# Kernel tuning notes

Hardware: AMD Instinct MI355X
Metric: run time of the kernel (lower is better)

## Reference

```python
import jax, jax.numpy as jnp
import numpy as np

KS = [3, 3, 7, 7, 11, 11, 21, 21]  # TEXT_KERNEL_SIZES
KMAX = 21
H = 8
D_MODEL = 1024
D_H = D_MODEL // H
R = 4
B = 2
N = 4096


def _extract_windows_1d(xh, k):
    # xh: (B, n, d_h) -> windows: (B, n, k, d_h), zero-padded, stride 1
    pad = k // 2
    xp = jnp.pad(xh, ((0, 0), (pad, pad), (0, 0)))
    idx = jnp.arange(xh.shape[1])[:, None] + jnp.arange(k)[None, :]  # (n, k)
    return xp[:, idx]  # (B, n, k, d_h)


def setup_inputs() -> dict:
    key = jax.random.key(0)
    ks = jax.random.split(key, 10)
    s = 0.02
    return {
        "x": jax.random.normal(ks[0], (B, N, D_MODEL), dtype=jnp.float32),
        "W_in": jax.random.normal(ks[1], (D_MODEL, D_MODEL), dtype=jnp.float32) * s,
        "b_in": jnp.zeros((D_MODEL,), dtype=jnp.float32),
        "W_out": jax.random.normal(ks[2], (D_MODEL, D_MODEL), dtype=jnp.float32) * (0.02 / np.sqrt(2.0 * 8)),
        "b_out": jnp.zeros((D_MODEL,), dtype=jnp.float32),
        "Wc": jax.random.normal(ks[3], (H, D_H, R), dtype=jnp.float32) * s,  # per-token coeff proj
        "A": jax.random.normal(ks[4], (H, R, KMAX), dtype=jnp.float32) * s,  # rank -> kernel-pos factor (padded to KMAX)
        "V": jax.random.normal(ks[5], (H, R, D_H), dtype=jnp.float32) * s,   # rank -> channel factor
        "base": jax.random.normal(ks[6], (H, KMAX, D_H), dtype=jnp.float32) * s,  # static kernel (padded)
        "alphas": jnp.zeros((H,), dtype=jnp.float32),  # sigmoid gate params
    }


def reference(x, W_in, b_in, W_out, b_out, Wc, A, V, base, alphas):
    Bsz, n, d = x.shape
    x_proj = x @ W_in.T + b_in                        # (B, n, d_model)
    x_heads = x_proj.reshape(Bsz, n, H, D_H)          # (B, n, H, d_h)
    head_outs = []
    for h in range(H):
        k = KS[h]
        x_h = x_heads[:, :, h, :]                     # (B, n, d_h)
        # Factored per-token kernel generation
        c = x_h @ Wc[h]                               # (B, n, R)
        dyn = jnp.einsum('bnr,rk,rd->bnkd', c, A[h, :, :k], V[h])  # (B, n, k, d_h)
        alpha = jax.nn.sigmoid(alphas[h])
        K_hat = alpha * dyn + (1.0 - alpha) * base[h, :k][None, None]  # (B, n, k, d_h)
        windows = _extract_windows_1d(x_h, k)         # (B, n, k, d_h)
        o_h = jnp.einsum('bnkd,bnkd->bnd', K_hat, windows)
        head_outs.append(o_h)
    concat = jnp.concatenate(head_outs, axis=-1)      # (B, n, d_model)
    return concat @ W_out.T + b_out
```

## Files before the change

kernel.cpp:

```cpp
#include <hip/hip_runtime.h>
#include <stdint.h>

typedef __bf16 bf16;
typedef __bf16 bf16x8 __attribute__((ext_vector_type(8)));
typedef float f32x4 __attribute__((ext_vector_type(4)));

#define AS1 __attribute__((address_space(1)))
#define AS3 __attribute__((address_space(3)))

__device__ __forceinline__ void gload_lds16(const void* g, void* l) {
    __builtin_amdgcn_global_load_lds((const AS1 uint32_t*)g, (AS3 uint32_t*)l, 16, 0, 0);
}

#define BM 128
#define BN 64
#define BK 64

template <typename OT>
__global__ __launch_bounds__(256, 4) void gemm_nt(
    const bf16* __restrict__ A, const bf16* __restrict__ B,
    const float* __restrict__ bias, OT* __restrict__ C,
    int M, int N, int K)
{
    __shared__ bf16 smA[BM * BK];
    __shared__ bf16 smB[BN * BK];

    const int tid  = threadIdx.x;
    const int wave = tid >> 6;
    const int lane = tid & 63;
    const int wm = (wave >> 1) * 64;
    const int wn = (wave & 1) * 32;
    const int rowA0 = blockIdx.x * BM;
    const int rowB0 = blockIdx.y * BN;

    f32x4 acc[4][2] = {};

    const int g  = lane >> 4;
    const int rm = lane & 15;

    for (int k0 = 0; k0 < K; k0 += BK) {
        #pragma unroll
        for (int i = 0; i < 4; ++i) {
            int slot = i * 256 + tid;
            int row  = slot >> 3;
            int kg   = slot & 7;
            int kd   = kg ^ ((row >> 1) & 7);
            gload_lds16(A + (size_t)(rowA0 + row) * K + k0 + kd * 8, &smA[slot * 8]);
        }
        #pragma unroll
        for (int i = 0; i < 2; ++i) {
            int slot = i * 256 + tid;
            int row  = slot >> 3;
            int kg   = slot & 7;
            int kd   = kg ^ ((row >> 1) & 7);
            gload_lds16(B + (size_t)(rowB0 + row) * K + k0 + kd * 8, &smB[slot * 8]);
        }
        __syncthreads();

        #pragma unroll
        for (int s = 0; s < 2; ++s) {
            bf16x8 af[4], bfr[2];
            #pragma unroll
            for (int mi = 0; mi < 4; ++mi) {
                int row  = wm + mi * 16 + rm;
                int slot = row * 8 + ((s * 4 + g) ^ ((row >> 1) & 7));
                af[mi] = *(const bf16x8*)&smA[slot * 8];
            }
            #pragma unroll
            for (int ni = 0; ni < 2; ++ni) {
                int row  = wn + ni * 16 + rm;
                int slot = row * 8 + ((s * 4 + g) ^ ((row >> 1) & 7));
                bfr[ni] = *(const bf16x8*)&smB[slot * 8];
            }
            #pragma unroll
            for (int mi = 0; mi < 4; ++mi)
                #pragma unroll
                for (int ni = 0; ni < 2; ++ni)
                    acc[mi][ni] = __builtin_amdgcn_mfma_f32_16x16x32_bf16(
                        af[mi], bfr[ni], acc[mi][ni], 0, 0, 0);
        }
        __syncthreads();
    }

    const int quad = lane >> 4;
    #pragma unroll
    for (int ni = 0; ni < 2; ++ni) {
        int col = rowB0 + wn + ni * 16 + rm;
        float bcol = bias[col];
        #pragma unroll
        for (int mi = 0; mi < 4; ++mi) {
            #pragma unroll
            for (int r = 0; r < 4; ++r) {
                int rowc = rowA0 + wm + mi * 16 + quad * 4 + r;
                C[(size_t)rowc * N + col] = (OT)(acc[mi][ni][r] + bcol);
            }
        }
    }
}

__global__ void cast_all_kernel(const float* __restrict__ x, bf16* __restrict__ xb,
                                const float* __restrict__ wi, bf16* __restrict__ wib,
                                const float* __restrict__ wo, bf16* __restrict__ wob)
{
    const int NX8 = (2 * 4096 * 1024) / 8;
    const int NW8 = (1024 * 1024) / 8;
    int i = blockIdx.x * 256 + threadIdx.x;
    const float* in; bf16* out; int idx;
    if (i < NX8)            { in = x;  out = xb;  idx = i; }
    else if (i < NX8 + NW8) { in = wi; out = wib; idx = i - NX8; }
    else                    { in = wo; out = wob; idx = i - NX8 - NW8; }
    const float4* p = (const float4*)in;
    float4 a = p[2 * idx], b = p[2 * idx + 1];
    bf16x8 o;
    o[0] = (bf16)a.x; o[1] = (bf16)a.y; o[2] = (bf16)a.z; o[3] = (bf16)a.w;
    o[4] = (bf16)b.x; o[5] = (bf16)b.y; o[6] = (bf16)b.z; o[7] = (bf16)b.w;
    *(bf16x8*)(out + 8 * idx) = o;
}

__global__ __launch_bounds__(256) void c_compute(
    const bf16* __restrict__ xpb, const float* __restrict__ Wc,
    float* __restrict__ cbuf)
{
    const int wave = threadIdx.x >> 6, lane = threadIdx.x & 63;
    const int row  = blockIdx.x * 4 + wave;
    const int h    = lane >> 3;
    const int d0   = (lane & 7) * 16;

    const bf16* xr = xpb + (size_t)row * 1024 + lane * 16;
    bf16x8 v0 = *(const bf16x8*)xr;
    bf16x8 v1 = *(const bf16x8*)(xr + 8);
    float p0 = 0.f, p1 = 0.f, p2 = 0.f, p3 = 0.f;
    #pragma unroll
    for (int i = 0; i < 16; ++i) {
        float xv = (i < 8) ? (float)v0[i & 7] : (float)v1[i & 7];
        float4 wr = *(const float4*)(Wc + h * 512 + (d0 + i) * 4);
        p0 += xv * wr.x; p1 += xv * wr.y; p2 += xv * wr.z; p3 += xv * wr.w;
    }
    #pragma unroll
    for (int off = 1; off <= 4; off <<= 1) {
        p0 += __shfl_xor(p0, off);
        p1 += __shfl_xor(p1, off);
        p2 += __shfl_xor(p2, off);
        p3 += __shfl_xor(p3, off);
    }
    if ((lane & 7) == 0) {
        float4 o = {p0, p1, p2, p3};
        *(float4*)(cbuf + (size_t)row * 32 + h * 4) = o;
    }
}

__constant__ int KS_c[8] = {3, 3, 7, 7, 11, 11, 21, 21};

template <int K>
__device__ __forceinline__ void mix_body5(
    int h, int tid, int r0, const bf16* __restrict__ xpb,
    const float* __restrict__ cbuf, const float* __restrict__ Aw,
    const float* __restrict__ Vw, const float* __restrict__ basew,
    float alpha, bf16* __restrict__ y, bf16* sx, float* sB)
{
    constexpr int T   = 8;
    constexpr int pad = K / 2;
    constexpr int R   = 16 + 2 * pad;
    constexpr int SX  = R * 16;
    constexpr int SB  = K * 32;

    #pragma unroll
    for (int p = 0; p < (SX + 255) / 256; ++p) {
        int slot = p * 256 + tid;
        if (slot < SX) {
            int lrow = slot >> 4;
            int grow = min(max(r0 - pad + lrow, 0), 8191);
            gload_lds16(xpb + (size_t)grow * 1024 + h * 128 + (slot & 15) * 8,
                        sx + slot * 8);
        }
    }
    #pragma unroll
    for (int p = 0; p < (SB + 255) / 256; ++p) {
        int slot = p * 256 + tid;
        if (slot < SB)
            gload_lds16(basew + h * 2688 + slot * 4, sB + slot * 4);
    }
    __syncthreads();

    const int d   = tid & 127;
    const int sub = tid >> 7;
    const int lr0 = sub * 8;
    const int nb  = (r0 & 4095) + sub * 8;

    float w[T + K - 1];
    #pragma unroll
    for (int j = 0; j < T + K - 1; ++j) {
        int nl = nb + j - pad;
        float v = (float)sx[(lr0 + j) * 128 + d];
        w[j] = (nl >= 0 && nl < 4096) ? v : 0.f;
    }

    float s0[T] = {}, s1[T] = {}, s2[T] = {}, s3[T] = {}, tv[T] = {};
    const float* Ah = Aw + h * 84;
    #pragma unroll
    for (int j = 0; j < K; ++j) {
        float a0 = Ah[j], a1 = Ah[21 + j], a2 = Ah[42 + j], a3 = Ah[63 + j];
        float bbj = sB[j * 128 + d];
        #pragma unroll
        for (int t = 0; t < T; ++t) {
            float x = w[t + j];
            s0[t] += a0 * x; s1[t] += a1 * x;
            s2[t] += a2 * x; s3[t] += a3 * x;
            tv[t] += bbj * x;
        }
    }

    float v0 = Vw[h * 512 + d],       v1 = Vw[h * 512 + 128 + d];
    float v2 = Vw[h * 512 + 256 + d], v3 = Vw[h * 512 + 384 + d];
    #pragma unroll
    for (int t = 0; t < T; ++t) {
        int rowo = r0 + sub * 8 + t;
        float4 c4 = *(const float4*)(cbuf + (size_t)rowo * 32 + h * 4);
        float o = alpha * (c4.x * v0 * s0[t] + c4.y * v1 * s1[t] +
                           c4.z * v2 * s2[t] + c4.w * v3 * s3[t])
                + (1.f - alpha) * tv[t];
        y[(size_t)rowo * 1024 + h * 128 + d] = (bf16)o;
    }
}

__global__ __launch_bounds__(256, 4) void head_mix5(
    const bf16* __restrict__ xpb, const float* __restrict__ cbuf,
    const float* __restrict__ Aw, const float* __restrict__ Vw,
    const float* __restrict__ basew, const float* __restrict__ alphas,
    bf16* __restrict__ y)
{
    __shared__ __align__(16) bf16  sx[36 * 128];
    __shared__ __align__(16) float sB[21 * 128];
    const int h  = blockIdx.y;
    const int r0 = blockIdx.x * 16;
    const float alpha = 1.f / (1.f + __expf(-alphas[h]));

    switch (KS_c[h]) {
        case 3:  mix_body5<3 >(h, threadIdx.x, r0, xpb, cbuf, Aw, Vw, basew, alpha, y, sx, sB); break;
        case 7:  mix_body5<7 >(h, threadIdx.x, r0, xpb, cbuf, Aw, Vw, basew, alpha, y, sx, sB); break;
        case 11: mix_body5<11>(h, threadIdx.x, r0, xpb, cbuf, Aw, Vw, basew, alpha, y, sx, sB); break;
        default: mix_body5<21>(h, threadIdx.x, r0, xpb, cbuf, Aw, Vw, basew, alpha, y, sx, sB); break;
    }
}

extern "C" void kernel_launch(void* const* d_in, const int* in_sizes, int n_in,
                              void* d_out, int out_size, void* d_ws, size_t ws_size,
                              hipStream_t stream)
{
    const float* x      = (const float*)d_in[0];
    const float* W_in   = (const float*)d_in[1];
    const float* b_in   = (const float*)d_in[2];
    const float* W_out  = (const float*)d_in[3];
    const float* b_out  = (const float*)d_in[4];
    const float* Wc     = (const float*)d_in[5];
    const float* Aw     = (const float*)d_in[6];
    const float* Vw     = (const float*)d_in[7];
    const float* basew  = (const float*)d_in[8];
    const float* alphas = (const float*)d_in[9];
    float* out = (float*)d_out;

    const size_t MB = 1u << 20;
    char* ws = (char*)d_ws;
    bf16*  xb   = (bf16*) (ws);
    bf16*  wib  = (bf16*) (ws + 16 * MB);
    bf16*  wob  = (bf16*) (ws + 18 * MB);
    bf16*  xpb  = (bf16*) (ws + 20 * MB);
    bf16*  yb   = (bf16*) (ws + 36 * MB);
    float* cbuf = (float*)(ws + 52 * MB);

    const int NTOT8 = (2 * 4096 * 1024 + 2 * 1024 * 1024) / 8;

    cast_all_kernel<<<NTOT8 / 256, 256, 0, stream>>>(x, xb, W_in, wib, W_out, wob);

    gemm_nt<bf16><<<dim3(8192 / BM, 1024 / BN), 256, 0, stream>>>(
        xb, wib, b_in, xpb, 8192, 1024, 1024);

    c_compute<<<8192 / 4, 256, 0, stream>>>(xpb, Wc, cbuf);

    head_mix5<<<dim3(512, 8), 256, 0, stream>>>(
        xpb, cbuf, Aw, Vw, basew, alphas, yb);

    gemm_nt<float><<<dim3(8192 / BM, 1024 / BN), 256, 0, stream>>>(
        yb, wob, b_out, out, 8192, 1024, 1024);
}
```

Measured before the change: 182.3 us.

## Widen GEMM tile to 128x128 and switch to 32x32x16 MFMA

Doubles the GEMM block N-tile from 64 to 128 so each wave computes a 64x64 sub-tile. It replaces the 16x16x32 bf16 MFMA with the 32x32x16 variant, adjusting LDS fragment indexing and the output row mapping. The aim is more reuse per LDS load and fewer MFMA issues per FLOP. In exchange, register pressure rises and occupancy drops (launch bounds go from 4 to 2), and the grid has fewer blocks.

```diff
diff --git a/kernel.cpp b/kernel.cpp
--- a/kernel.cpp
+++ b/kernel.cpp
@@ -4,6 +4,7 @@
 typedef __bf16 bf16;
 typedef __bf16 bf16x8 __attribute__((ext_vector_type(8)));
 typedef float f32x4 __attribute__((ext_vector_type(4)));
+typedef float f32x16 __attribute__((ext_vector_type(16)));
 
 #define AS1 __attribute__((address_space(1)))
 #define AS3 __attribute__((address_space(3)))
@@ -13,11 +14,11 @@
 }
 
 #define BM 128
-#define BN 64
+#define BN 128
 #define BK 64
 
 template <typename OT>
-__global__ __launch_bounds__(256, 4) void gemm_nt(
+__global__ __launch_bounds__(256, 2) void gemm_nt(
     const bf16* __restrict__ A, const bf16* __restrict__ B,
     const float* __restrict__ bias, OT* __restrict__ C,
     int M, int N, int K)
@@ -29,14 +30,14 @@
     const int wave = tid >> 6;
     const int lane = tid & 63;
     const int wm = (wave >> 1) * 64;
-    const int wn = (wave & 1) * 32;
+    const int wn = (wave & 1) * 64;
     const int rowA0 = blockIdx.x * BM;
     const int rowB0 = blockIdx.y * BN;
 
-    f32x4 acc[4][2] = {};
-
-    const int g  = lane >> 4;
-    const int rm = lane & 15;
+    f32x16 acc[2][2] = {};
+
+    const int l31 = lane & 31;
+    const int khi = lane >> 5;
 
     for (int k0 = 0; k0 < K; k0 += BK) {
         #pragma unroll
@@ -46,52 +47,45 @@
             int kg   = slot & 7;
             int kd   = kg ^ ((row >> 1) & 7);
             gload_lds16(A + (size_t)(rowA0 + row) * K + k0 + kd * 8, &smA[slot * 8]);
-        }
-        #pragma unroll
-        for (int i = 0; i < 2; ++i) {
-            int slot = i * 256 + tid;
-            int row  = slot >> 3;
-            int kg   = slot & 7;
-            int kd   = kg ^ ((row >> 1) & 7);
             gload_lds16(B + (size_t)(rowB0 + row) * K + k0 + kd * 8, &smB[slot * 8]);
         }
         __syncthreads();
 
         #pragma unroll
-        for (int s = 0; s < 2; ++s) {
-            bf16x8 af[4], bfr[2];
-            #pragma unroll
-            for (int mi = 0; mi < 4; ++mi) {
-                int row  = wm + mi * 16 + rm;
-                int slot = row * 8 + ((s * 4 + g) ^ ((row >> 1) & 7));
+        for (int s = 0; s < 4; ++s) {
+            bf16x8 af[2], bfr[2];
+            #pragma unroll
+            for (int mi = 0; mi < 2; ++mi) {
+                int row  = wm + mi * 32 + l31;
+                int slot = row * 8 + ((s * 2 + khi) ^ ((row >> 1) & 7));
                 af[mi] = *(const bf16x8*)&smA[slot * 8];
             }
             #pragma unroll
             for (int ni = 0; ni < 2; ++ni) {
-                int row  = wn + ni * 16 + rm;
-                int slot = row * 8 + ((s * 4 + g) ^ ((row >> 1) & 7));
+                int row  = wn + ni * 32 + l31;
+                int slot = row * 8 + ((s * 2 + khi) ^ ((row >> 1) & 7));
                 bfr[ni] = *(const bf16x8*)&smB[slot * 8];
             }
             #pragma unroll
-            for (int mi = 0; mi < 4; ++mi)
+            for (int mi = 0; mi < 2; ++mi)
                 #pragma unroll
                 for (int ni = 0; ni < 2; ++ni)
-                    acc[mi][ni] = __builtin_amdgcn_mfma_f32_16x16x32_bf16(
+                    acc[mi][ni] = __builtin_amdgcn_mfma_f32_32x32x16_bf16(
                         af[mi], bfr[ni], acc[mi][ni], 0, 0, 0);
         }
         __syncthreads();
     }
 
-    const int quad = lane >> 4;
     #pragma unroll
     for (int ni = 0; ni < 2; ++ni) {
-        int col = rowB0 + wn + ni * 16 + rm;
+        int col = rowB0 + wn + ni * 32 + l31;
         float bcol = bias[col];
         #pragma unroll
-        for (int mi = 0; mi < 4; ++mi) {
-            #pragma unroll
-            for (int r = 0; r < 4; ++r) {
-                int rowc = rowA0 + wm + mi * 16 + quad * 4 + r;
+        for (int mi = 0; mi < 2; ++mi) {
+            #pragma unroll
+            for (int r = 0; r < 16; ++r) {
+                int row32 = (r & 3) + 8 * (r >> 2) + 4 * khi;
+                int rowc  = rowA0 + wm + mi * 32 + row32;
                 C[(size_t)rowc * N + col] = (OT)(acc[mi][ni][r] + bcol);
             }
         }
```

After: 179.8 us. Within noise of the previous version (-1.4%).
